# Kernel tuning notes

Measured on AMD Instinct MI355X. Metric: run time of the kernel, lower is better.

## Reference

```python
import jax, jax.numpy as jnp
import numpy as np
import math

C = 256
N_HEAD = 8
GROUPS = 16
EPS = 1e-5


def group_norm(x, w, b):
    # x: [B, C, H, W]; biased variance over (group_channels, H, W), like torch GroupNorm
    B, Cc, H, W = x.shape
    xg = x.reshape(B, GROUPS, Cc // GROUPS, H, W)
    mean = xg.mean(axis=(2, 3, 4), keepdims=True)
    var = ((xg - mean) ** 2).mean(axis=(2, 3, 4), keepdims=True)
    xn = ((xg - mean) * jax.lax.rsqrt(var + EPS)).reshape(B, Cc, H, W)
    return xn * w[None, :, None, None] + b[None, :, None, None]


def setup_inputs() -> dict:
    key = jax.random.key(0)
    k0, k1, k2, k3, k4, k5 = jax.random.split(key, 6)
    B, H, W = 4, 48, 48
    input_feat = jax.random.normal(k0, (B, C, H, W), dtype=jnp.float32)
    gn_weight = jnp.ones((C,), dtype=jnp.float32) + 0.02 * jax.random.normal(k1, (C,), dtype=jnp.float32)
    gn_bias = 0.02 * jax.random.normal(k2, (C,), dtype=jnp.float32)
    w_qkv = jax.random.normal(k3, (3 * C, C), dtype=jnp.float32) / math.sqrt(C)  # Conv2d 1x1, no bias
    w_out = jax.random.normal(k4, (C, C), dtype=jnp.float32) / math.sqrt(C)      # Conv2d 1x1
    b_out = 0.02 * jax.random.normal(k5, (C,), dtype=jnp.float32)
    return {"input_feat": input_feat, "gn_weight": gn_weight, "gn_bias": gn_bias,
            "w_qkv": w_qkv, "w_out": w_out, "b_out": b_out}


def reference(input_feat, gn_weight, gn_bias, w_qkv, w_out, b_out):
    # H=W=48 <= max_attn_size=48 -> full attention branch
    B, Cc, H, W = input_feat.shape
    n, d = N_HEAD, Cc // N_HEAD
    S = H * W
    normed = group_norm(input_feat, gn_weight, gn_bias)
    # 1x1 conv QKV: [B, 3C, H, W]
    qkv = jnp.einsum('oc,bchw->bohw', w_qkv, normed)
    # view(B, n, 3*d, H, W).chunk(3, dim=2) == reshape to (B, n, 3, d, S)
    qkv = qkv.reshape(B, n, 3, d, S)
    q, k, v = qkv[:, :, 0], qkv[:, :, 1], qkv[:, :, 2]  # each [B, n, d, S]
    # NOTE: original divides by sqrt(channel), not sqrt(head_dim)
    scale = 1.0 / math.sqrt(Cc)
    scores = jnp.einsum('bnds,bndt->bnst', q, k) * scale  # [B, n, S, S]
    attn = jax.nn.softmax(scores, axis=-1)
    o = jnp.einsum('bnst,bndt->bnds', attn, v)  # [B, n, d, S]
    o = o.reshape(B, Cc, H, W)
    out = jnp.einsum('oc,bchw->bohw', w_out, o) + b_out[None, :, None, None]
    return out + input_feat
```

## Files before the change

kernel.cpp:

```cpp
#include <hip/hip_runtime.h>
#include <hip/hip_bf16.h>
#include <stdint.h>

#define S    2304
#define CHN  256
#define BATCH 4
#define NKEYS 1152
#define QS   0.09016844005556021f

typedef __attribute__((ext_vector_type(8))) short bf16x8;
typedef __attribute__((ext_vector_type(4))) short bf16x4;
typedef __attribute__((ext_vector_type(4))) float f32x4;
typedef __attribute__((ext_vector_type(4))) uint32_t u32x4;
typedef __attribute__((ext_vector_type(4))) unsigned short u16x4;
typedef unsigned short u16;

#define AS1 __attribute__((address_space(1)))
#define AS3 __attribute__((address_space(3)))
#define GLDS(gptr, lptr) __builtin_amdgcn_global_load_lds((const AS1 void*)(gptr), (AS3 void*)(lptr), 16, 0, 0)

__device__ __forceinline__ u16 f2bf(float f) {
  union { float f; uint32_t u; } v; v.f = f;
  uint32_t u = v.u;
  u += 0x7fffu + ((u >> 16) & 1u);
  return (u16)(u >> 16);
}
__device__ __forceinline__ float bf2f(u16 h) {
  union { uint32_t u; float f; } v; v.u = ((uint32_t)h) << 16;
  return v.f;
}
__device__ __forceinline__ uint32_t pk_bf16(float a, float b) {
  union { __hip_bfloat162 h; uint32_t u; } cv;
  cv.h = __float22bfloat162_rn(make_float2(a, b));
  return cv.u;
}

__global__ void k_gnstats(const float* __restrict__ x,
                          const float* __restrict__ wq, const float* __restrict__ wo,
                          u16* __restrict__ wq_bf, u16* __restrict__ wo_bf,
                          float* __restrict__ sraw) {
  int blk = blockIdx.x;
  int bg = blk >> 2, part = blk & 3;
  const float4* p = (const float4*)(x + (size_t)bg * 36864) + part * 2304;
  float s = 0.f, ss = 0.f;
  for (int i = threadIdx.x; i < 2304; i += 256) {
    float4 v = p[i];
    s  += v.x + v.y + v.z + v.w;
    ss += v.x * v.x + v.y * v.y + v.z * v.z + v.w * v.w;
  }
  int lane = threadIdx.x & 63, wv = threadIdx.x >> 6;
  for (int m = 1; m < 64; m <<= 1) { s += __shfl_xor(s, m, 64); ss += __shfl_xor(ss, m, 64); }
  __shared__ float rs[4], rss[4];
  if (lane == 0) { rs[wv] = s; rss[wv] = ss; }
  __syncthreads();
  if (threadIdx.x == 0) {
    sraw[blk * 2]     = rs[0] + rs[1] + rs[2] + rs[3];
    sraw[blk * 2 + 1] = rss[0] + rss[1] + rss[2] + rss[3];
  }
  int gid = blk * 256 + threadIdx.x;
  #pragma unroll
  for (int it = 0; it < 3; ++it) {
    int i = gid + it * 65536;
    wq_bf[i] = f2bf(wq[i]);
  }
  wo_bf[gid] = f2bf(wo[gid]);
}

__global__ void k_gnnorm(const float* __restrict__ x, const float* __restrict__ w,
                         const float* __restrict__ bias, const float* __restrict__ sraw,
                         u16* __restrict__ nt) {
  int bid = blockIdx.x;
  int b = bid / 144, r = bid % 144;
  int sblk = r >> 2, cq = r & 3;
  int t = threadIdx.x;
  int ni = t & 63, cgrp = t >> 6;
  int s = sblk * 64 + ni;
  int cbase = cq * 64 + cgrp * 16;
  int bgi = b * 16 + (cbase >> 4);
  float sx  = sraw[bgi * 8]     + sraw[bgi * 8 + 2] + sraw[bgi * 8 + 4] + sraw[bgi * 8 + 6];
  float ssx = sraw[bgi * 8 + 1] + sraw[bgi * 8 + 3] + sraw[bgi * 8 + 5] + sraw[bgi * 8 + 7];
  float mean = sx * (1.f / 36864.f);
  float var  = ssx * (1.f / 36864.f) - mean * mean;
  float rstd = rsqrtf(var + 1e-5f);
  bf16x8 v0, v1;
  #pragma unroll
  for (int e = 0; e < 16; ++e) {
    int c = cbase + e;
    float val = x[(size_t)(b * 256 + c) * S + s];
    float xn = (val - mean) * rstd * w[c] + bias[c];
    if (e < 8) v0[e] = (short)f2bf(xn); else v1[e - 8] = (short)f2bf(xn);
  }
  u16* dst = nt + (size_t)(b * S + s) * 256 + cbase;
  *(bf16x8*)dst = v0;
  *(bf16x8*)(dst + 8) = v1;
}

__global__ __launch_bounds__(256) void k_qkv(const u16* __restrict__ A,
                                             const u16* __restrict__ Bm,
                                             u16* __restrict__ qkt,
                                             u16* __restrict__ vt) {
  __shared__ __align__(16) u16 As[2][64 * 32];
  __shared__ __align__(16) u16 Bs[2][128 * 32];
  int tid = threadIdx.x, lane = tid & 63, w = tid >> 6;
  int wr = w >> 1, wc = w & 1;
  int cb = lane & 15, q4 = lane >> 4;
  int m0 = blockIdx.y * 64, n0 = blockIdx.x * 128;

  const u16* gA0 = A  + (size_t)(m0 + (tid >> 2)) * 256 + (tid & 3) * 8;
  const u16* gB0 = Bm + (size_t)(n0 + (tid >> 2)) * 256 + (tid & 3) * 8;
  const u16* gB1 = gB0 + 64 * 256;
  char* lA = (char*)&As[0][0] + (w << 10);
  char* lB = (char*)&Bs[0][0] + (w << 10);

  #define STAGE_Q(buf, k0) do {                      \
    GLDS(gA0 + (k0), lA + (buf) * 4096);             \
    GLDS(gB0 + (k0), lB + (buf) * 8192);             \
    GLDS(gB1 + (k0), lB + (buf) * 8192 + 4096);      \
  } while (0)

  f32x4 zero4 = {0.f, 0.f, 0.f, 0.f};
  f32x4 acc[2][4];
  for (int i = 0; i < 2; ++i) for (int j = 0; j < 4; ++j) acc[i][j] = zero4;

  STAGE_Q(0, 0);
  __syncthreads();
  for (int ks = 0; ks < 8; ++ks) {
    int cur = ks & 1;
    if (ks < 7) STAGE_Q(cur ^ 1, (ks + 1) * 32);
    const u16* as = &As[cur][0];
    const u16* bs = &Bs[cur][0];
    bf16x8 af[2], bfr[4];
    for (int i = 0; i < 2; ++i)
      af[i]  = *(const bf16x8*)&as[(wr * 32 + i * 16 + cb) * 32 + 8 * q4];
    for (int j = 0; j < 4; ++j)
      bfr[j] = *(const bf16x8*)&bs[(wc * 64 + j * 16 + cb) * 32 + 8 * q4];
    for (int i = 0; i < 2; ++i)
      for (int j = 0; j < 4; ++j)
        acc[i][j] = __builtin_amdgcn_mfma_f32_16x16x32_bf16(af[i], bfr[j], acc[i][j], 0, 0, 0);
    __syncthreads();
  }

  for (int i = 0; i < 2; ++i)
    for (int j = 0; j < 4; ++j) {
      int ob = m0 + wr * 32 + i * 16 + q4 * 4;
      int n  = n0 + wc * 64 + j * 16 + cb;
      int h = ob / 96, oq = ob % 96;
      if (oq < 64) {
        float sc = (oq < 32) ? QS : 1.f;
        u16x4 pk;
        for (int r = 0; r < 4; ++r) pk[r] = f2bf(acc[i][j][r] * sc);
        *(u16x4*)&qkt[(size_t)n * 512 + h * 64 + oq] = pk;
      } else {
        for (int r = 0; r < 4; ++r)
          vt[(size_t)(h * 32 + oq - 64 + r) * 9216 + n] = f2bf(acc[i][j][r]);
      }
    }
  #undef STAGE_Q
}

__global__ __launch_bounds__(512) void k_attn(const u16* __restrict__ qkt,
                                              const u16* __restrict__ vt,
                                              u16* __restrict__ ot) {
  __shared__ __align__(16) u16 Ks[2][2][2048];
  __shared__ __align__(16) u16 Vd[2][2][2048];
  __shared__ float Ls[8][16];

  int tid = threadIdx.x, lane = tid & 63, w = tid >> 6;
  int cb = lane & 15, g4 = lane >> 4;
  int qw = w & 3, half = w >> 2;
  int hw = blockIdx.x;
  int orig = (hw & 7) * 144 + (hw >> 3);
  int bh = orig / 36, qtile = orig % 36;
  int b = bh >> 3, h = bh & 7;
  int q0 = qtile * 64 + qw * 16;

  const u16* kbase = qkt + (size_t)(b * S) * 512 + h * 64 + 32 + (size_t)half * NKEYS * 512;
  const u16* vbase = vt + (size_t)(h * 32) * 9216 + (size_t)b * S + half * NKEYS;

  bf16x8 qf = *(const bf16x8*)&qkt[(size_t)(b * S + q0 + cb) * 512 + h * 64 + 8 * g4];
  bf16x8 vones;
  #pragma unroll
  for (int e = 0; e < 8; ++e) vones[e] = (short)0x3F80;

  f32x4 zero4 = {0.f, 0.f, 0.f, 0.f};
  f32x4 acc_o[2]; acc_o[0] = zero4; acc_o[1] = zero4;
  f32x4 lacc4 = zero4;

  int xk = (cb ^ (cb >> 2)) & 3;

  const u16* p_k = &Ks[half][0][cb * 32 + ((g4 ^ xk) * 8)];
  const u16* p_v[2][2];
  #pragma unroll
  for (int kk = 0; kk < 2; ++kk)
    #pragma unroll
    for (int h2 = 0; h2 < 2; ++h2) {
      int chunk = 4 * kk + 2 * h2 + (g4 >> 1);
      p_v[kk][h2] = &Vd[half][0][cb * 64 + ((chunk ^ (cb & 7)) << 3) + 4 * (g4 & 1)];
    }

  int tloc = tid & 255;
  int krow = tloc >> 2, kch = (tloc & 3) ^ ((krow ^ (krow >> 2)) & 3);
  int vrow = tloc >> 3, vch = (tloc & 7) ^ (vrow & 7);
  const u16* gK = kbase + (size_t)krow * 512 + kch * 8;
  const u16* gV = vbase + (size_t)vrow * 9216 + vch * 8;
  char* ldsK = (char*)&Ks[half][0][0] + (qw << 10);
  char* ldsV = (char*)&Vd[half][0][0] + (qw << 10);

  #define STAGE_A(buf) do {                          \
    GLDS(gK, ldsK + (buf) * 4096);                   \
    GLDS(gV, ldsV + (buf) * 4096);                   \
    gK += 64 * 512; gV += 64;                        \
  } while (0)

  #define TILE(buf, pf) do {                                                   \
    if (pf) STAGE_A(buf ^ 1);                                                  \
    bf16x8 kf[4];                                                              \
    _Pragma("unroll")                                                          \
    for (int k4 = 0; k4 < 4; ++k4)                                             \
      kf[k4] = *(const bf16x8*)(p_k + (buf) * 2048 + k4 * 512);                \
    bf16x4 vlo[2][2], vhi[2][2];                                 \
    _Pragma("unroll")                                                          \
    for (int jd = 0; jd < 2; ++jd)                                             \
      _Pragma("unroll")                                                        \
      for (int kk = 0; kk < 2; ++kk) {                                         \
        vlo[jd][kk] = *(const bf16x4*)(p_v[kk][0] + (buf) * 2048 + jd * 1024); \
        vhi[jd][kk] = *(const bf16x4*)(p_v[kk][1] + (buf) * 2048 + jd * 1024); \
      }                                                                        \
    f32x4 pacc[4];                                                             \
    __builtin_amdgcn_s_setprio(1);                                             \
    _Pragma("unroll")                                                          \
    for (int k4 = 0; k4 < 4; ++k4)                                             \
      pacc[k4] = __builtin_amdgcn_mfma_f32_16x16x32_bf16(kf[k4], qf, zero4, 0, 0, 0); \
    __builtin_amdgcn_s_setprio(0);                                             \
    uint32_t W01[4], W23[4];                                                   \
    _Pragma("unroll")                                                          \
    for (int k4 = 0; k4 < 4; ++k4) {                                           \
      f32x4 p = pacc[k4];                                                      \
      float e0 = __builtin_amdgcn_exp2f(p[0]);                                 \
      float e1 = __builtin_amdgcn_exp2f(p[1]);                                 \
      float e2 = __builtin_amdgcn_exp2f(p[2]);                                 \
      float e3 = __builtin_amdgcn_exp2f(p[3]);                                 \
      W01[k4] = pk_bf16(e0, e1);                                               \
      W23[k4] = pk_bf16(e2, e3);                                               \
    }                                                                          \
    union { u32x4 u; bf16x8 v; } pu0, pu1;                                     \
    pu0.u = (u32x4){W01[0], W23[0], W01[1], W23[1]};                           \
    pu1.u = (u32x4){W01[2], W23[2], W01[3], W23[3]};                           \
    __builtin_amdgcn_s_setprio(1);                                             \
    lacc4 = __builtin_amdgcn_mfma_f32_16x16x32_bf16(pu0.v, vones, lacc4, 0, 0, 0); \
    lacc4 = __builtin_amdgcn_mfma_f32_16x16x32_bf16(pu1.v, vones, lacc4, 0, 0, 0); \
    _Pragma("unroll")                                                          \
    for (int jd = 0; jd < 2; ++jd) {                                           \
      bf16x8 vb0 = __builtin_shufflevector(vlo[jd][0], vhi[jd][0], 0,1,2,3,4,5,6,7); \
      bf16x8 vb1 = __builtin_shufflevector(vlo[jd][1], vhi[jd][1], 0,1,2,3,4,5,6,7); \
      acc_o[jd] = __builtin_amdgcn_mfma_f32_16x16x32_bf16(pu0.v, vb0, acc_o[jd], 0, 0, 0); \
      acc_o[jd] = __builtin_amdgcn_mfma_f32_16x16x32_bf16(pu1.v, vb1, acc_o[jd], 0, 0, 0); \
    }                                                                          \
    __builtin_amdgcn_s_setprio(0);                                             \
    __syncthreads();                                                           \
  } while (0)

  STAGE_A(0);
  __syncthreads();
  for (int it = 0; it < 9; ++it) {
    TILE(0, 1);
    TILE(1, it < 8);
  }

  float* OsF = (float*)&Ks[0][0][0];
  float* myO = OsF + w * 512;
  #pragma unroll
  for (int jd = 0; jd < 2; ++jd)
    *(f32x4*)&myO[(cb + 16 * jd) * 16 + 4 * g4] = acc_o[jd];
  if (cb == 0)
    *(f32x4*)&Ls[w][4 * g4] = lacc4;
  __syncthreads();

  const float* A0 = OsF + qw * 512;
  const float* A1 = OsF + (qw + 4) * 512;
  int dd = half * 16 + cb;
  f32x4 s0 = *(const f32x4*)&A0[dd * 16 + 4 * g4];
  f32x4 s1 = *(const f32x4*)&A1[dd * 16 + 4 * g4];
  f32x4 lt0 = *(const f32x4*)&Ls[qw][4 * g4];
  f32x4 lt1 = *(const f32x4*)&Ls[qw + 4][4 * g4];
  #pragma unroll
  for (int r = 0; r < 4; ++r) {
    float inv = __builtin_amdgcn_rcpf(lt0[r] + lt1[r]);
    int sq = q0 + 4 * g4 + r;
    ot[(size_t)(b * S + sq) * 256 + h * 32 + dd] = f2bf((s0[r] + s1[r]) * inv);
  }
  #undef STAGE_A
  #undef TILE
}

__global__ __launch_bounds__(256) void k_oproj(const u16* __restrict__ A,
                                               const u16* __restrict__ Bm,
                                               float* __restrict__ out,
                                               const float* __restrict__ bias,
                                               const float* __restrict__ resid) {
  __shared__ __align__(16) u16 As[2][64 * 32];
  __shared__ __align__(16) u16 Bs[2][64 * 32];
  int tid = threadIdx.x, lane = tid & 63, w = tid >> 6;
  int cb = lane & 15, q4 = lane >> 4;
  int m0 = blockIdx.y * 64, n0 = blockIdx.x * 64;

  const u16* gA0 = A  + (size_t)(m0 + (tid >> 2)) * 256 + (tid & 3) * 8;
  const u16* gB0 = Bm + (size_t)(n0 + (tid >> 2)) * 256 + (tid & 3) * 8;
  char* lA = (char*)&As[0][0] + (w << 10);
  char* lB = (char*)&Bs[0][0] + (w << 10);

  #define STAGE_O(buf, k0) do {                      \
    GLDS(gA0 + (k0), lA + (buf) * 4096);             \
    GLDS(gB0 + (k0), lB + (buf) * 4096);             \
  } while (0)

  f32x4 zero4 = {0.f, 0.f, 0.f, 0.f};
  f32x4 acc[4];
  for (int j = 0; j < 4; ++j) acc[j] = zero4;

  STAGE_O(0, 0);
  __syncthreads();
  for (int ks = 0; ks < 8; ++ks) {
    int cur = ks & 1;
    if (ks < 7) STAGE_O(cur ^ 1, (ks + 1) * 32);
    const u16* as = &As[cur][0];
    const u16* bs = &Bs[cur][0];
    bf16x8 af = *(const bf16x8*)&as[(w * 16 + cb) * 32 + 8 * q4];
    bf16x8 bfr[4];
    for (int j = 0; j < 4; ++j)
      bfr[j] = *(const bf16x8*)&bs[(j * 16 + cb) * 32 + 8 * q4];
    for (int j = 0; j < 4; ++j)
      acc[j] = __builtin_amdgcn_mfma_f32_16x16x32_bf16(af, bfr[j], acc[j], 0, 0, 0);
    __syncthreads();
  }

  for (int j = 0; j < 4; ++j)
    for (int r = 0; r < 4; ++r) {
      int o = m0 + w * 16 + q4 * 4 + r;
      int n = n0 + j * 16 + cb;
      int b = n / S, s2 = n % S;
      size_t gi = (size_t)(b * 256 + o) * S + s2;
      out[gi] = acc[j][r] + bias[o] + resid[gi];
    }
  #undef STAGE_O
}

extern "C" void kernel_launch(void* const* d_in, const int* in_sizes, int n_in,
                              void* d_out, int out_size, void* d_ws, size_t ws_size,
                              hipStream_t stream) {
  const float* input = (const float*)d_in[0];
  const float* gnw   = (const float*)d_in[1];
  const float* gnb   = (const float*)d_in[2];
  const float* wqkv  = (const float*)d_in[3];
  const float* wout  = (const float*)d_in[4];
  const float* bout  = (const float*)d_in[5];
  float* out = (float*)d_out;
  char* ws = (char*)d_ws;

  size_t o_wq  = 0;
  size_t o_wo  = o_wq + (size_t)768 * 256 * 2;
  size_t o_st  = o_wo + (size_t)256 * 256 * 2;
  size_t o_nt  = o_st + 2048;
  size_t o_qkt = o_nt + (size_t)9216 * 256 * 2;
  size_t o_vt  = o_qkt + (size_t)9216 * 512 * 2;

  u16*    wq_bf = (u16*)(ws + o_wq);
  u16*    wo_bf = (u16*)(ws + o_wo);
  float*  sraw  = (float*)(ws + o_st);
  u16*    nt    = (u16*)(ws + o_nt);
  u16*    qkt   = (u16*)(ws + o_qkt);
  u16*    vt    = (u16*)(ws + o_vt);
  u16*    otb   = (u16*)(ws + o_nt);

  k_gnstats<<<256, 256, 0, stream>>>(input, wqkv, wout, wq_bf, wo_bf, sraw);
  k_gnnorm<<<576, 256, 0, stream>>>(input, gnw, gnb, sraw, nt);
  k_qkv<<<dim3(72, 12), 256, 0, stream>>>(wq_bf, nt, qkt, vt);
  k_attn<<<1152, 512, 0, stream>>>(qkt, vt, otb);
  k_oproj<<<dim3(144, 4), 256, 0, stream>>>(wo_bf, otb, out, bout, input);
}
```

Before: 82.99 us.

## Halve attention block to 256 threads with two query tiles per wave

The attention kernel now runs 256 threads per block instead of 512. Each wave handles 32 queries as two 16-row sub-tiles, so every K/V fragment loaded from LDS feeds twice as many MFMAs. Each thread issues two global-to-LDS loads per tile to keep the staging volume the same, and the final cross-half reduction uses a padded scratch layout split across the K and V buffers. The aim is to cut LDS read traffic and barrier cost per unit of work, at the price of more registers per wave and fewer waves available to hide latency.

```diff
diff --git a/kernel.cpp b/kernel.cpp
--- a/kernel.cpp
+++ b/kernel.cpp
@@ -158,33 +158,37 @@
   #undef STAGE_Q
 }
 
-__global__ __launch_bounds__(512) void k_attn(const u16* __restrict__ qkt,
-                                              const u16* __restrict__ vt,
-                                              u16* __restrict__ ot) {
+__global__ __launch_bounds__(256, 4) void k_attn(const u16* __restrict__ qkt,
+                                                 const u16* __restrict__ vt,
+                                                 u16* __restrict__ ot) {
   __shared__ __align__(16) u16 Ks[2][2][2048];
   __shared__ __align__(16) u16 Vd[2][2][2048];
-  __shared__ float Ls[8][16];
+  __shared__ float Ls[2][2][32];
 
   int tid = threadIdx.x, lane = tid & 63, w = tid >> 6;
   int cb = lane & 15, g4 = lane >> 4;
-  int qw = w & 3, half = w >> 2;
+  int qw = w & 1, half = w >> 1;
   int hw = blockIdx.x;
   int orig = (hw & 7) * 144 + (hw >> 3);
   int bh = orig / 36, qtile = orig % 36;
   int b = bh >> 3, h = bh & 7;
-  int q0 = qtile * 64 + qw * 16;
+  int q0 = qtile * 64 + qw * 32;
 
   const u16* kbase = qkt + (size_t)(b * S) * 512 + h * 64 + 32 + (size_t)half * NKEYS * 512;
   const u16* vbase = vt + (size_t)(h * 32) * 9216 + (size_t)b * S + half * NKEYS;
 
-  bf16x8 qf = *(const bf16x8*)&qkt[(size_t)(b * S + q0 + cb) * 512 + h * 64 + 8 * g4];
+  bf16x8 qf[2];
+  #pragma unroll
+  for (int qi = 0; qi < 2; ++qi)
+    qf[qi] = *(const bf16x8*)&qkt[(size_t)(b * S + q0 + 16 * qi + cb) * 512 + h * 64 + 8 * g4];
   bf16x8 vones;
   #pragma unroll
   for (int e = 0; e < 8; ++e) vones[e] = (short)0x3F80;
 
   f32x4 zero4 = {0.f, 0.f, 0.f, 0.f};
-  f32x4 acc_o[2]; acc_o[0] = zero4; acc_o[1] = zero4;
-  f32x4 lacc4 = zero4;
+  f32x4 acc_o[2][2];
+  acc_o[0][0] = zero4; acc_o[0][1] = zero4; acc_o[1][0] = zero4; acc_o[1][1] = zero4;
+  f32x4 lacc4[2]; lacc4[0] = zero4; lacc4[1] = zero4;
 
   int xk = (cb ^ (cb >> 2)) & 3;
 
@@ -198,18 +202,26 @@
       p_v[kk][h2] = &Vd[half][0][cb * 64 + ((chunk ^ (cb & 7)) << 3) + 4 * (g4 & 1)];
     }
 
-  int tloc = tid & 255;
-  int krow = tloc >> 2, kch = (tloc & 3) ^ ((krow ^ (krow >> 2)) & 3);
-  int vrow = tloc >> 3, vch = (tloc & 7) ^ (vrow & 7);
-  const u16* gK = kbase + (size_t)krow * 512 + kch * 8;
-  const u16* gV = vbase + (size_t)vrow * 9216 + vch * 8;
-  char* ldsK = (char*)&Ks[half][0][0] + (qw << 10);
-  char* ldsV = (char*)&Vd[half][0][0] + (qw << 10);
+  int ww = w & 1;
+  int c1 = ww * 64 + lane, c2 = c1 + 128;
+  int kr1 = c1 >> 2, kc1 = (c1 & 3) ^ ((kr1 ^ (kr1 >> 2)) & 3);
+  int kr2 = c2 >> 2, kc2 = (c2 & 3) ^ ((kr2 ^ (kr2 >> 2)) & 3);
+  int vr1 = c1 >> 3, vc1 = (c1 & 7) ^ (vr1 & 7);
+  int vr2 = c2 >> 3, vc2 = (c2 & 7) ^ (vr2 & 7);
+  const u16* gK1 = kbase + (size_t)kr1 * 512 + kc1 * 8;
+  const u16* gK2 = kbase + (size_t)kr2 * 512 + kc2 * 8;
+  const u16* gV1 = vbase + (size_t)vr1 * 9216 + vc1 * 8;
+  const u16* gV2 = vbase + (size_t)vr2 * 9216 + vc2 * 8;
+  char* ldsK = (char*)&Ks[half][0][0] + (ww << 10);
+  char* ldsV = (char*)&Vd[half][0][0] + (ww << 10);
 
   #define STAGE_A(buf) do {                          \
-    GLDS(gK, ldsK + (buf) * 4096);                   \
-    GLDS(gV, ldsV + (buf) * 4096);                   \
-    gK += 64 * 512; gV += 64;                        \
+    GLDS(gK1, ldsK + (buf) * 4096);                  \
+    GLDS(gK2, ldsK + (buf) * 4096 + 2048);           \
+    GLDS(gV1, ldsV + (buf) * 4096);                  \
+    GLDS(gV2, ldsV + (buf) * 4096 + 2048);           \
+    gK1 += 64 * 512; gK2 += 64 * 512;                \
+    gV1 += 64; gV2 += 64;                            \
   } while (0)
 
   #define TILE(buf, pf) do {                                                   \
@@ -218,7 +230,7 @@
     _Pragma("unroll")                                                          \
     for (int k4 = 0; k4 < 4; ++k4)                                             \
       kf[k4] = *(const bf16x8*)(p_k + (buf) * 2048 + k4 * 512);                \
-    bf16x4 vlo[2][2], vhi[2][2];                                 \
+    bf16x4 vlo[2][2], vhi[2][2];              \
     _Pragma("unroll")                                                          \
     for (int jd = 0; jd < 2; ++jd)                                             \
       _Pragma("unroll")                                                        \
@@ -226,37 +238,40 @@
         vlo[jd][kk] = *(const bf16x4*)(p_v[kk][0] + (buf) * 2048 + jd * 1024); \
         vhi[jd][kk] = *(const bf16x4*)(p_v[kk][1] + (buf) * 2048 + jd * 1024); \
       }                                                                        \
-    f32x4 pacc[4];                                                             \
-    __builtin_amdgcn_s_setprio(1);                                             \
     _Pragma("unroll")                                                          \
-    for (int k4 = 0; k4 < 4; ++k4)                                             \
-      pacc[k4] = __builtin_amdgcn_mfma_f32_16x16x32_bf16(kf[k4], qf, zero4, 0, 0, 0); \
-    __builtin_amdgcn_s_setprio(0);                                             \
-    uint32_t W01[4], W23[4];                                                   \
-    _Pragma("unroll")                                                          \
-    for (int k4 = 0; k4 < 4; ++k4) {                                           \
-      f32x4 p = pacc[k4];                                                      \
-      float e0 = __builtin_amdgcn_exp2f(p[0]);                                 \
-      float e1 = __builtin_amdgcn_exp2f(p[1]);                                 \
-      float e2 = __builtin_amdgcn_exp2f(p[2]);                                 \
-      float e3 = __builtin_amdgcn_exp2f(p[3]);                                 \
-      W01[k4] = pk_bf16(e0, e1);                                               \
-      W23[k4] = pk_bf16(e2, e3);                                               \
+    for (int qi = 0; qi < 2; ++qi) {                                           \
+      f32x4 pacc[4];                                                           \
+      __builtin_amdgcn_s_setprio(1);                                           \
+      _Pragma("unroll")                                                        \
+      for (int k4 = 0; k4 < 4; ++k4)                                           \
+        pacc[k4] = __builtin_amdgcn_mfma_f32_16x16x32_bf16(kf[k4], qf[qi], zero4, 0, 0, 0); \
+      __builtin_amdgcn_s_setprio(0);                                           \
+      uint32_t W01[4], W23[4];                                                 \
+      _Pragma("unroll")                                                        \
+      for (int k4 = 0; k4 < 4; ++k4) {                                         \
+        f32x4 p = pacc[k4];                                                    \
+        float e0 = __builtin_amdgcn_exp2f(p[0]);                               \
+        float e1 = __builtin_amdgcn_exp2f(p[1]);                               \
+        float e2 = __builtin_amdgcn_exp2f(p[2]);                               \
+        float e3 = __builtin_amdgcn_exp2f(p[3]);                               \
+        W01[k4] = pk_bf16(e0, e1);                                             \
+        W23[k4] = pk_bf16(e2, e3);                                             \
+      }                                                                        \
+      union { u32x4 u; bf16x8 v; } pu0, pu1;                                   \
+      pu0.u = (u32x4){W01[0], W23[0], W01[1], W23[1]};                         \
+      pu1.u = (u32x4){W01[2], W23[2], W01[3], W23[3]};                         \
+      __builtin_amdgcn_s_setprio(1);                                           \
+      lacc4[qi] = __builtin_amdgcn_mfma_f32_16x16x32_bf16(pu0.v, vones, lacc4[qi], 0, 0, 0); \
+      lacc4[qi] = __builtin_amdgcn_mfma_f32_16x16x32_bf16(pu1.v, vones, lacc4[qi], 0, 0, 0); \
+      _Pragma("unroll")                                                        \
+      for (int jd = 0; jd < 2; ++jd) {                                         \
+        bf16x8 vb0 = __builtin_shufflevector(vlo[jd][0], vhi[jd][0], 0,1,2,3,4,5,6,7); \
+        bf16x8 vb1 = __builtin_shufflevector(vlo[jd][1], vhi[jd][1], 0,1,2,3,4,5,6,7); \
+        acc_o[qi][jd] = __builtin_amdgcn_mfma_f32_16x16x32_bf16(pu0.v, vb0, acc_o[qi][jd], 0, 0, 0); \
+        acc_o[qi][jd] = __builtin_amdgcn_mfma_f32_16x16x32_bf16(pu1.v, vb1, acc_o[qi][jd], 0, 0, 0); \
+      }                                                                        \
+      __builtin_amdgcn_s_setprio(0);                                           \
     }                                                                          \
-    union { u32x4 u; bf16x8 v; } pu0, pu1;                                     \
-    pu0.u = (u32x4){W01[0], W23[0], W01[1], W23[1]};                           \
-    pu1.u = (u32x4){W01[2], W23[2], W01[3], W23[3]};                           \
-    __builtin_amdgcn_s_setprio(1);                                             \
-    lacc4 = __builtin_amdgcn_mfma_f32_16x16x32_bf16(pu0.v, vones, lacc4, 0, 0, 0); \
-    lacc4 = __builtin_amdgcn_mfma_f32_16x16x32_bf16(pu1.v, vones, lacc4, 0, 0, 0); \
-    _Pragma("unroll")                                                          \
-    for (int jd = 0; jd < 2; ++jd) {                                           \
-      bf16x8 vb0 = __builtin_shufflevector(vlo[jd][0], vhi[jd][0], 0,1,2,3,4,5,6,7); \
-      bf16x8 vb1 = __builtin_shufflevector(vlo[jd][1], vhi[jd][1], 0,1,2,3,4,5,6,7); \
-      acc_o[jd] = __builtin_amdgcn_mfma_f32_16x16x32_bf16(pu0.v, vb0, acc_o[jd], 0, 0, 0); \
-      acc_o[jd] = __builtin_amdgcn_mfma_f32_16x16x32_bf16(pu1.v, vb1, acc_o[jd], 0, 0, 0); \
-    }                                                                          \
-    __builtin_amdgcn_s_setprio(0);                                             \
     __syncthreads();                                                           \
   } while (0)
 
@@ -267,27 +282,36 @@
     TILE(1, it < 8);
   }
 
-  float* OsF = (float*)&Ks[0][0][0];
-  float* myO = OsF + w * 512;
-  #pragma unroll
-  for (int jd = 0; jd < 2; ++jd)
-    *(f32x4*)&myO[(cb + 16 * jd) * 16 + 4 * g4] = acc_o[jd];
-  if (cb == 0)
-    *(f32x4*)&Ls[w][4 * g4] = lacc4;
+  float* scrK = (float*)&Ks[0][0][0];
+  float* scrV = (float*)&Vd[0][0][0];
+  int reg = qw * 2 + half;
+  float* myS = (reg < 2 ? scrK : scrV) + (reg & 1) * 1152;
+  #pragma unroll
+  for (int qi = 0; qi < 2; ++qi)
+    #pragma unroll
+    for (int jd = 0; jd < 2; ++jd)
+      *(f32x4*)&myS[(cb + 16 * jd) * 36 + 16 * qi + 4 * g4] = acc_o[qi][jd];
+  if (cb == 0) {
+    *(f32x4*)&Ls[qw][half][4 * g4] = lacc4[0];
+    *(f32x4*)&Ls[qw][half][16 + 4 * g4] = lacc4[1];
+  }
   __syncthreads();
 
-  const float* A0 = OsF + qw * 512;
-  const float* A1 = OsF + (qw + 4) * 512;
+  const float* s0p = (qw == 0 ? scrK : scrV);
+  const float* s1p = s0p + 1152;
   int dd = half * 16 + cb;
-  f32x4 s0 = *(const f32x4*)&A0[dd * 16 + 4 * g4];
-  f32x4 s1 = *(const f32x4*)&A1[dd * 16 + 4 * g4];
-  f32x4 lt0 = *(const f32x4*)&Ls[qw][4 * g4];
-  f32x4 lt1 = *(const f32x4*)&Ls[qw + 4][4 * g4];
-  #pragma unroll
-  for (int r = 0; r < 4; ++r) {
-    float inv = __builtin_amdgcn_rcpf(lt0[r] + lt1[r]);
-    int sq = q0 + 4 * g4 + r;
-    ot[(size_t)(b * S + sq) * 256 + h * 32 + dd] = f2bf((s0[r] + s1[r]) * inv);
+  #pragma unroll
+  for (int qi2 = 0; qi2 < 2; ++qi2) {
+    f32x4 s0 = *(const f32x4*)&s0p[dd * 36 + 16 * qi2 + 4 * g4];
+    f32x4 s1 = *(const f32x4*)&s1p[dd * 36 + 16 * qi2 + 4 * g4];
+    f32x4 lt0 = *(const f32x4*)&Ls[qw][0][16 * qi2 + 4 * g4];
+    f32x4 lt1 = *(const f32x4*)&Ls[qw][1][16 * qi2 + 4 * g4];
+    #pragma unroll
+    for (int r = 0; r < 4; ++r) {
+      float inv = __builtin_amdgcn_rcpf(lt0[r] + lt1[r]);
+      int sq = q0 + 16 * qi2 + 4 * g4 + r;
+      ot[(size_t)(b * S + sq) * 256 + h * 32 + dd] = f2bf((s0[r] + s1[r]) * inv);
+    }
   }
   #undef STAGE_A
   #undef TILE
@@ -375,6 +399,6 @@
   k_gnstats<<<256, 256, 0, stream>>>(input, wqkv, wout, wq_bf, wo_bf, sraw);
   k_gnnorm<<<576, 256, 0, stream>>>(input, gnw, gnb, sraw, nt);
   k_qkv<<<dim3(72, 12), 256, 0, stream>>>(wq_bf, nt, qkt, vt);
-  k_attn<<<1152, 512, 0, stream>>>(qkt, vt, otb);
+  k_attn<<<1152, 256, 0, stream>>>(qkt, vt, otb);
   k_oproj<<<dim3(144, 4), 256, 0, stream>>>(wo_bf, otb, out, bout, input);
 }
```

Measured after the change: 80.28 us. -3.3%, faster.
